# Kernel optimization log

Hardware: AMD Instinct MI355X
Metric: run time of the kernel (lower is better)

## Reference

```python
import jax, jax.numpy as jnp
import numpy as np

B, K, D = 32768, 32, 128

def setup_inputs() -> dict:
    key = jax.random.key(0)
    k1, k2, k3, k4, k5, k6 = jax.random.split(key, 6)
    s = 1.0 / np.sqrt(D)
    return {
        "h_ego": jax.random.normal(k1, (B, D), jnp.float32),
        "h_nei": jax.random.normal(k2, (B, K, D), jnp.float32),
        "nbr_mask": jax.random.randint(k3, (B, K), 0, 2, jnp.int32),
        "W_msg": jax.random.normal(k4, (D, D), jnp.float32) * s,
        "W_attn": jax.random.normal(k5, (1, 2 * D), jnp.float32) * s,
        "W_self": jax.random.normal(k6, (D, D), jnp.float32) * s,
        "b_self": jnp.zeros((D,), jnp.float32),
    }

def reference(h_ego, h_nei, nbr_mask, W_msg, W_attn, W_self, b_self):
    # msg_proj (nn.Linear, no bias): y = x @ W.T
    nbr_proj = jnp.einsum('bkd,ed->bke', h_nei, W_msg)          # [B,K,D]
    ego_proj = jnp.einsum('bd,ed->be', h_ego, W_msg)            # [B,D]
    # additive scorer on [ego_proj || nbr_proj]: split W_attn into two halves
    a = W_attn[0]                                               # [2D]
    a_ego, a_nbr = a[:D], a[D:]
    logits = ego_proj @ a_ego[:, None]                          # [B,1]
    logits = logits + jnp.einsum('bkd,d->bk', nbr_proj, a_nbr)  # [B,K]
    logits = jax.nn.leaky_relu(logits, negative_slope=0.2)
    logits = jnp.where(nbr_mask > 0, logits, -jnp.inf)
    attn = jax.nn.softmax(logits, axis=1)                       # [B,K]
    attn = jnp.where(jnp.isfinite(attn), attn, 0.0)
    nbr_message = jnp.einsum('bkd,bk->bd', nbr_proj, attn)      # [B,D]
    self_loop = h_ego @ W_self.T + b_self                       # [B,D]
    return jnp.tanh(nbr_message + self_loop)
```

## Files before the change

### kernel.cpp

```cpp
#include <hip/hip_runtime.h>
#include <hip/hip_bf16.h>
#include <math.h>

#define B_ROWS 32768
#define KNBR 32
#define DDIM 128

#define WS_VEGO 0
#define WS_VNBR 128
#define WS_WMT  256
#define WS_WST  (256 + 128*128)

__global__ __launch_bounds__(256) void prep_kernel(
    const float* __restrict__ W_msg, const float* __restrict__ W_attn,
    const float* __restrict__ W_self, float* __restrict__ ws) {
    int t = threadIdx.x;
    int gid = blockIdx.x * 256 + t;
    if (gid < 128 * 128) {
        int e = gid >> 7, d = gid & 127;
        ws[WS_WMT + d * 128 + e] = W_msg[e * 128 + d];
        ws[WS_WST + d * 128 + e] = W_self[e * 128 + d];
    }
    if (blockIdx.x == 0 && t < 128) {
        float ve = 0.f, vn = 0.f;
        for (int e = 0; e < 128; ++e) {
            float w = W_msg[e * 128 + t];
            ve += W_attn[e] * w;
            vn += W_attn[128 + e] * w;
        }
        ws[WS_VEGO + t] = ve;
        ws[WS_VNBR + t] = vn;
    }
}

__global__ __launch_bounds__(256) void attn_kernel(
    const float* __restrict__ h_ego, const float* __restrict__ h_nei,
    const int* __restrict__ nbr_mask, const float* __restrict__ ws,
    float* __restrict__ hbar_out) {
    int t = threadIdx.x;
    int w = t >> 6, l = t & 63;
    long b = (long)blockIdx.x * 4 + w;

    float2 vn2 = ((const float2*)(ws + WS_VNBR))[l];
    float2 ve2 = ((const float2*)(ws + WS_VEGO))[l];
    float2 he2 = ((const float2*)(h_ego + b * DDIM))[l];

    const float2* row = (const float2*)(h_nei + b * (KNBR * DDIM));
    float2 hreg[KNBR];
#pragma unroll
    for (int k = 0; k < KNBR; ++k) hreg[k] = row[k * 64 + l];

    int mv = nbr_mask[b * KNBR + (l & 31)];
    unsigned long long bal = __ballot((l < KNBR) && (mv > 0));
    unsigned vmask = (unsigned)bal;

    float pe = he2.x * ve2.x + he2.y * ve2.y;
#pragma unroll
    for (int s = 32; s; s >>= 1) pe += __shfl_xor(pe, s, 64);

    float e[KNBR];
    float m = -INFINITY;
#pragma unroll
    for (int k = 0; k < KNBR; ++k) {
        float p = hreg[k].x * vn2.x + hreg[k].y * vn2.y;
#pragma unroll
        for (int s = 32; s; s >>= 1) p += __shfl_xor(p, s, 64);
        p += pe;
        p = p > 0.f ? p : 0.2f * p;
        p = ((vmask >> k) & 1u) ? p : -INFINITY;
        e[k] = p;
        m = fmaxf(m, p);
    }
    float ssum = 0.f;
#pragma unroll
    for (int k = 0; k < KNBR; ++k) {
        float ev = ((vmask >> k) & 1u) ? __expf(e[k] - m) : 0.f;
        e[k] = ev;
        ssum += ev;
    }
    float inv = ssum > 0.f ? 1.f / ssum : 0.f;

    float2 acc = make_float2(0.f, 0.f);
#pragma unroll
    for (int k = 0; k < KNBR; ++k) {
        acc.x += e[k] * hreg[k].x;
        acc.y += e[k] * hreg[k].y;
    }
    acc.x *= inv;
    acc.y *= inv;
    ((float2*)(hbar_out + b * DDIM))[l] = acc;
}

__global__ __launch_bounds__(256) void out_kernel(
    const float* __restrict__ h_ego, const float* __restrict__ ws,
    const float* __restrict__ b_self, float* __restrict__ out) {
    __shared__ float xh[32 * DDIM];
    __shared__ float xe[32 * DDIM];

    int t = threadIdx.x;
    long rbase = (long)blockIdx.x * 32;

    const float4* srcH = (const float4*)(out + rbase * DDIM);
    const float4* srcE = (const float4*)(h_ego + rbase * DDIM);
#pragma unroll
    for (int i = 0; i < 4; ++i) {
        ((float4*)xh)[i * 256 + t] = srcH[i * 256 + t];
        ((float4*)xe)[i * 256 + t] = srcE[i * 256 + t];
    }
    __syncthreads();

    const float4* WmT = (const float4*)(ws + WS_WMT);
    const float4* WsT = (const float4*)(ws + WS_WST);
    int tc = t & 31;
    int tr = t >> 5;

    float acc[4][4] = {{0.f}};
    for (int d = 0; d < 128; ++d) {
        float4 wm = WmT[d * 32 + tc];
        float4 wsv = WsT[d * 32 + tc];
#pragma unroll
        for (int r = 0; r < 4; ++r) {
            float a = xh[(tr * 4 + r) * DDIM + d];
            float bb = xe[(tr * 4 + r) * DDIM + d];
            acc[r][0] += a * wm.x + bb * wsv.x;
            acc[r][1] += a * wm.y + bb * wsv.y;
            acc[r][2] += a * wm.z + bb * wsv.z;
            acc[r][3] += a * wm.w + bb * wsv.w;
        }
    }

    float4 bv = ((const float4*)b_self)[tc];
#pragma unroll
    for (int r = 0; r < 4; ++r) {
        float4 o;
        o.x = tanhf(acc[r][0] + bv.x);
        o.y = tanhf(acc[r][1] + bv.y);
        o.z = tanhf(acc[r][2] + bv.z);
        o.w = tanhf(acc[r][3] + bv.w);
        ((float4*)(out + (rbase + tr * 4 + r) * DDIM))[tc] = o;
    }
}

extern "C" void kernel_launch(void* const* d_in, const int* in_sizes, int n_in,
                              void* d_out, int out_size, void* d_ws, size_t ws_size,
                              hipStream_t stream) {
    const float* h_ego   = (const float*)d_in[0];
    const float* h_nei   = (const float*)d_in[1];
    const int*   nbr_mask= (const int*)d_in[2];
    const float* W_msg   = (const float*)d_in[3];
    const float* W_attn  = (const float*)d_in[4];
    const float* W_self  = (const float*)d_in[5];
    const float* b_self  = (const float*)d_in[6];
    float* out = (float*)d_out;
    float* ws  = (float*)d_ws;

    prep_kernel<<<64, 256, 0, stream>>>(W_msg, W_attn, W_self, ws);
    attn_kernel<<<B_ROWS / 4, 256, 0, stream>>>(h_ego, h_nei, nbr_mask, ws, out);
    out_kernel<<<B_ROWS / 32, 256, 0, stream>>>(h_ego, ws, b_self, out);
}
```

Measured before the change: 754.8 us.

## Fuse attention aggregation and output projection into one kernel via shared memory

Merges the attention kernel and the output GEMM kernel so each block computes the attention-weighted neighbor sums for its 32 rows directly into shared memory, then runs the projection and tanh from there. This removes the global write and re-read of the intermediate hbar buffer and one kernel launch. The GEMM inner loop is also changed to read float4 from shared memory and process four d-steps per iteration. In exchange, each block now has only 1024 blocks total with each wave handling 8 rows serially, which lowers the number of in-flight h_nei loads and may hurt latency hiding on the bandwidth-bound attention phase.

```diff
diff --git a/kernel.cpp b/kernel.cpp
--- a/kernel.cpp
+++ b/kernel.cpp
@@ -1,5 +1,4 @@
 #include <hip/hip_runtime.h>
-#include <hip/hip_bf16.h>
 #include <math.h>
 
 #define B_ROWS 32768
@@ -33,99 +32,109 @@
     }
 }
 
-__global__ __launch_bounds__(256) void attn_kernel(
+__global__ __launch_bounds__(256) void fused_kernel(
     const float* __restrict__ h_ego, const float* __restrict__ h_nei,
     const int* __restrict__ nbr_mask, const float* __restrict__ ws,
-    float* __restrict__ hbar_out) {
-    int t = threadIdx.x;
-    int w = t >> 6, l = t & 63;
-    long b = (long)blockIdx.x * 4 + w;
-
-    float2 vn2 = ((const float2*)(ws + WS_VNBR))[l];
-    float2 ve2 = ((const float2*)(ws + WS_VEGO))[l];
-    float2 he2 = ((const float2*)(h_ego + b * DDIM))[l];
-
-    const float2* row = (const float2*)(h_nei + b * (KNBR * DDIM));
-    float2 hreg[KNBR];
-#pragma unroll
-    for (int k = 0; k < KNBR; ++k) hreg[k] = row[k * 64 + l];
-
-    int mv = nbr_mask[b * KNBR + (l & 31)];
-    unsigned long long bal = __ballot((l < KNBR) && (mv > 0));
-    unsigned vmask = (unsigned)bal;
-
-    float pe = he2.x * ve2.x + he2.y * ve2.y;
-#pragma unroll
-    for (int s = 32; s; s >>= 1) pe += __shfl_xor(pe, s, 64);
-
-    float e[KNBR];
-    float m = -INFINITY;
-#pragma unroll
-    for (int k = 0; k < KNBR; ++k) {
-        float p = hreg[k].x * vn2.x + hreg[k].y * vn2.y;
-#pragma unroll
-        for (int s = 32; s; s >>= 1) p += __shfl_xor(p, s, 64);
-        p += pe;
-        p = p > 0.f ? p : 0.2f * p;
-        p = ((vmask >> k) & 1u) ? p : -INFINITY;
-        e[k] = p;
-        m = fmaxf(m, p);
-    }
-    float ssum = 0.f;
-#pragma unroll
-    for (int k = 0; k < KNBR; ++k) {
-        float ev = ((vmask >> k) & 1u) ? __expf(e[k] - m) : 0.f;
-        e[k] = ev;
-        ssum += ev;
-    }
-    float inv = ssum > 0.f ? 1.f / ssum : 0.f;
-
-    float2 acc = make_float2(0.f, 0.f);
-#pragma unroll
-    for (int k = 0; k < KNBR; ++k) {
-        acc.x += e[k] * hreg[k].x;
-        acc.y += e[k] * hreg[k].y;
-    }
-    acc.x *= inv;
-    acc.y *= inv;
-    ((float2*)(hbar_out + b * DDIM))[l] = acc;
-}
-
-__global__ __launch_bounds__(256) void out_kernel(
-    const float* __restrict__ h_ego, const float* __restrict__ ws,
     const float* __restrict__ b_self, float* __restrict__ out) {
     __shared__ float xh[32 * DDIM];
     __shared__ float xe[32 * DDIM];
 
     int t = threadIdx.x;
+    int w = t >> 6, l = t & 63;
     long rbase = (long)blockIdx.x * 32;
 
-    const float4* srcH = (const float4*)(out + rbase * DDIM);
     const float4* srcE = (const float4*)(h_ego + rbase * DDIM);
 #pragma unroll
     for (int i = 0; i < 4; ++i) {
-        ((float4*)xh)[i * 256 + t] = srcH[i * 256 + t];
         ((float4*)xe)[i * 256 + t] = srcE[i * 256 + t];
+    }
+
+    float2 vn2 = ((const float2*)(ws + WS_VNBR))[l];
+    float2 ve2 = ((const float2*)(ws + WS_VEGO))[l];
+    __syncthreads();
+
+    for (int i = 0; i < 8; ++i) {
+        int row = w * 8 + i;
+        long b = rbase + row;
+
+        float2 he2 = ((const float2*)xe)[row * 64 + l];
+
+        const float2* rowp = (const float2*)(h_nei + b * (KNBR * DDIM));
+        float2 hreg[KNBR];
+#pragma unroll
+        for (int k = 0; k < KNBR; ++k) hreg[k] = rowp[k * 64 + l];
+
+        int mv = nbr_mask[b * KNBR + (l & 31)];
+        unsigned long long bal = __ballot((l < KNBR) && (mv > 0));
+        unsigned vmask = (unsigned)bal;
+
+        float pe = he2.x * ve2.x + he2.y * ve2.y;
+#pragma unroll
+        for (int s = 32; s; s >>= 1) pe += __shfl_xor(pe, s, 64);
+
+        float e[KNBR];
+        float m = -INFINITY;
+#pragma unroll
+        for (int k = 0; k < KNBR; ++k) {
+            float p = hreg[k].x * vn2.x + hreg[k].y * vn2.y;
+#pragma unroll
+            for (int s = 32; s; s >>= 1) p += __shfl_xor(p, s, 64);
+            p += pe;
+            p = p > 0.f ? p : 0.2f * p;
+            p = ((vmask >> k) & 1u) ? p : -INFINITY;
+            e[k] = p;
+            m = fmaxf(m, p);
+        }
+        float ssum = 0.f;
+#pragma unroll
+        for (int k = 0; k < KNBR; ++k) {
+            float ev = ((vmask >> k) & 1u) ? __expf(e[k] - m) : 0.f;
+            e[k] = ev;
+            ssum += ev;
+        }
+        float inv = ssum > 0.f ? 1.f / ssum : 0.f;
+
+        float2 acc = make_float2(0.f, 0.f);
+#pragma unroll
+        for (int k = 0; k < KNBR; ++k) {
+            acc.x += e[k] * hreg[k].x;
+            acc.y += e[k] * hreg[k].y;
+        }
+        acc.x *= inv;
+        acc.y *= inv;
+        ((float2*)xh)[row * 64 + l] = acc;
     }
     __syncthreads();
 
     const float4* WmT = (const float4*)(ws + WS_WMT);
     const float4* WsT = (const float4*)(ws + WS_WST);
+    const float4* xh4 = (const float4*)xh;
+    const float4* xe4 = (const float4*)xe;
     int tc = t & 31;
     int tr = t >> 5;
 
     float acc[4][4] = {{0.f}};
-    for (int d = 0; d < 128; ++d) {
-        float4 wm = WmT[d * 32 + tc];
-        float4 wsv = WsT[d * 32 + tc];
+    for (int d4 = 0; d4 < 32; ++d4) {
+        float4 wm0 = WmT[(d4 * 4 + 0) * 32 + tc];
+        float4 wm1 = WmT[(d4 * 4 + 1) * 32 + tc];
+        float4 wm2 = WmT[(d4 * 4 + 2) * 32 + tc];
+        float4 wm3 = WmT[(d4 * 4 + 3) * 32 + tc];
+        float4 ws0 = WsT[(d4 * 4 + 0) * 32 + tc];
+        float4 ws1 = WsT[(d4 * 4 + 1) * 32 + tc];
+        float4 ws2 = WsT[(d4 * 4 + 2) * 32 + tc];
+        float4 ws3 = WsT[(d4 * 4 + 3) * 32 + tc];
 #pragma unroll
         for (int r = 0; r < 4; ++r) {
-            float a = xh[(tr * 4 + r) * DDIM + d];
-            float bb = xe[(tr * 4 + r) * DDIM + d];
-            acc[r][0] += a * wm.x + bb * wsv.x;
-            acc[r][1] += a * wm.y + bb * wsv.y;
-            acc[r][2] += a * wm.z + bb * wsv.z;
-            acc[r][3] += a * wm.w + bb * wsv.w;
+            float4 a = xh4[(tr * 4 + r) * 32 + d4];
+            float4 g = xe4[(tr * 4 + r) * 32 + d4];
+            acc[r][0] += a.x * wm0.x + a.y * wm1.x + a.z * wm2.x + a.w * wm3.x
+                       + g.x * ws0.x + g.y * ws1.x + g.z * ws2.x + g.w * ws3.x;
+            acc[r][1] += a.x * wm0.y + a.y * wm1.y + a.z * wm2.y + a.w * wm3.y
+                       + g.x * ws0.y + g.y * ws1.y + g.z * ws2.y + g.w * ws3.y;
+            acc[r][2] += a.x * wm0.z + a.y * wm1.z + a.z * wm2.z + a.w * wm3.z
+                       + g.x * ws0.z + g.y * ws1.z + g.z * ws2.z + g.w * ws3.z;
+            acc[r][3] += a.x * wm0.w + a.y * wm1.w + a.z * wm2.w + a.w * wm3.w
+                       + g.x * ws0.w + g.y * ws1.w + g.z * ws2.w + g.w * ws3.w;
         }
     }
 
@@ -155,6 +164,6 @@
     float* ws  = (float*)d_ws;
 
     prep_kernel<<<64, 256, 0, stream>>>(W_msg, W_attn, W_self, ws);
-    attn_kernel<<<B_ROWS / 4, 256, 0, stream>>>(h_ego, h_nei, nbr_mask, ws, out);
-    out_kernel<<<B_ROWS / 32, 256, 0, stream>>>(h_ego, ws, b_self, out);
+    fused_kernel<<<B_ROWS / 32, 256, 0, stream>>>(h_ego, h_nei, nbr_mask, ws,
+                                                  b_self, out);
 }
```

Result: faster. 739.0 us (-2.1%).
